# Kernel tuning notes

Measured on AMD Instinct MI355X. Metric: run time of the kernel, lower is better.

## Reference

```python
import jax, jax.numpy as jnp
import numpy as np

NL, NK = 10000, 2000          # ligand / keypoint node counts
ELL, EKL = 320000, 160000     # lig->lig and kp->lig edge counts
IN, HID, OUT = 128, 128, 128  # in_size, hidden_size, out_size
FDIM = 2 * IN + 1             # edge MLP input: [h_src, h_dst, dij]


def silu(x):
    return x * jax.nn.sigmoid(x)


def setup_inputs() -> dict:
    keys = iter(jax.random.split(jax.random.key(0), 64))

    def nrm(shape, scale=0.02):
        return jax.random.normal(next(keys), shape, dtype=jnp.float32) * scale

    d = {}
    d["h_lig"] = jax.random.normal(next(keys), (NL, IN), dtype=jnp.float32)
    d["h_kp"] = jax.random.normal(next(keys), (NK, IN), dtype=jnp.float32)
    d["x_lig"] = jax.random.normal(next(keys), (NL, 3), dtype=jnp.float32)
    d["x_kp"] = jax.random.normal(next(keys), (NK, 3), dtype=jnp.float32)
    # per-node normalizer (e.g. neighbor count); keep >= 1 to avoid blowup
    d["z_lig"] = jax.random.uniform(next(keys), (NL, 1), dtype=jnp.float32, minval=1.0, maxval=32.0)
    for e in ("ll", "kl"):
        d[e + "_eW1"] = nrm((FDIM, HID)); d[e + "_eb1"] = jnp.zeros((HID,), jnp.float32)
        d[e + "_eW2"] = nrm((HID, HID)); d[e + "_eb2"] = jnp.zeros((HID,), jnp.float32)
        d[e + "_aW"] = nrm((HID, 1)); d[e + "_ab"] = jnp.zeros((1,), jnp.float32)
        d[e + "_cW1"] = nrm((FDIM, HID)); d[e + "_cb1"] = jnp.zeros((HID,), jnp.float32)
        d[e + "_cW2"] = nrm((HID, HID)); d[e + "_cb2"] = jnp.zeros((HID,), jnp.float32)
        d[e + "_cW3"] = nrm((HID, 1), scale=0.001)  # xavier gain=0.001 final coord layer
    d["n_W1"] = nrm((IN + HID, HID)); d["n_b1"] = jnp.zeros((HID,), jnp.float32)
    d["n_W2"] = nrm((HID, OUT)); d["n_b2"] = jnp.zeros((OUT,), jnp.float32)
    d["ll_src"] = jax.random.randint(next(keys), (ELL,), 0, NL, dtype=jnp.int32)
    d["ll_dst"] = jax.random.randint(next(keys), (ELL,), 0, NL, dtype=jnp.int32)
    d["kl_src"] = jax.random.randint(next(keys), (EKL,), 0, NK, dtype=jnp.int32)
    d["kl_dst"] = jax.random.randint(next(keys), (EKL,), 0, NL, dtype=jnp.int32)
    return d


def _edge_messages(hs, hd, xs, xd, eW1, eb1, eW2, eb2, aW, ab, cW1, cb1, cW2, cb2, cW3):
    x_diff = xs - xd                                     # fn.u_sub_v
    dij = jnp.linalg.norm(x_diff, axis=1, keepdims=True)  # [E,1]
    x_diff = x_diff / (dij + 1.0)
    f = jnp.concatenate([hs, hd, dij], axis=1)           # [E, 2*IN+1]
    m = silu(f @ eW1 + eb1)
    m = silu(m @ eW2 + eb2)
    msg_h = m * jax.nn.sigmoid(m @ aW + ab)              # soft attention gate
    c = silu(f @ cW1 + cb1)
    c = silu(c @ cW2 + cb2)
    msg_x = (c @ cW3) * x_diff                           # use_tanh=False path
    return msg_h, msg_x


def reference(h_lig, h_kp, x_lig, x_kp, z_lig,
              ll_eW1, ll_eb1, ll_eW2, ll_eb2, ll_aW, ll_ab,
              ll_cW1, ll_cb1, ll_cW2, ll_cb2, ll_cW3,
              kl_eW1, kl_eb1, kl_eW2, kl_eb2, kl_aW, kl_ab,
              kl_cW1, kl_cb1, kl_cW2, kl_cb2, kl_cW3,
              n_W1, n_b1, n_W2, n_b2,
              ll_src, ll_dst, kl_src, kl_dst):
    # lig -> lig edges
    mh_ll, mx_ll = _edge_messages(h_lig[ll_src], h_lig[ll_dst], x_lig[ll_src], x_lig[ll_dst],
                                  ll_eW1, ll_eb1, ll_eW2, ll_eb2, ll_aW, ll_ab,
                                  ll_cW1, ll_cb1, ll_cW2, ll_cb2, ll_cW3)
    # kp -> lig edges
    mh_kl, mx_kl = _edge_messages(h_kp[kl_src], h_lig[kl_dst], x_kp[kl_src], x_lig[kl_dst],
                                  kl_eW1, kl_eb1, kl_eW2, kl_eb2, kl_aW, kl_ab,
                                  kl_cW1, kl_cb1, kl_cW2, kl_cb2, kl_cW3)
    nl = h_lig.shape[0]
    # multi_update_all with cross_reducer='sum', then per-node normalization by z
    h_neigh = (jax.ops.segment_sum(mh_ll, ll_dst, num_segments=nl)
               + jax.ops.segment_sum(mh_kl, kl_dst, num_segments=nl)) / z_lig
    x_neigh = (jax.ops.segment_sum(mx_ll, ll_dst, num_segments=nl)
               + jax.ops.segment_sum(mx_kl, kl_dst, num_segments=nl)) / z_lig
    nin = jnp.concatenate([h_lig, h_neigh], axis=1)
    h_out = h_lig + (silu(nin @ n_W1 + n_b1) @ n_W2 + n_b2)  # norm=False -> Identity
    x_out = x_lig + x_neigh
    return (h_out, x_out)
```

## Files before the change

### kernel.cpp

```cpp
#include <hip/hip_runtime.h>
#include <hip/hip_bf16.h>
#include <math.h>

#define EPB  32
#define MSTR 136
#define FSTR 264

typedef __attribute__((ext_vector_type(8))) short short8;
typedef __attribute__((ext_vector_type(4))) float f32x4;

__device__ __forceinline__ unsigned short f2bf(float x) {
    unsigned int u = __float_as_uint(x);
    u += 0x7fffu + ((u >> 16) & 1u);
    return (unsigned short)(u >> 16);
}
__device__ __forceinline__ float bf2f(short v) {
    return __uint_as_float(((unsigned int)(unsigned short)v) << 16);
}
__device__ __forceinline__ unsigned int pkbf(float a, float b) {
    __hip_bfloat162 h = __float22bfloat162_rn(make_float2(a, b));
    union { __hip_bfloat162 h2; unsigned int u; } cv; cv.h2 = h; return cv.u;
}
__device__ __forceinline__ float frcp(float x) { return __builtin_amdgcn_rcpf(x); }
__device__ __forceinline__ float fsilu(float x) {
    return x * frcp(1.0f + __expf(-x));
}
__device__ __forceinline__ float fsigm(float x) {
    return frcp(1.0f + __expf(-x));
}
__device__ __forceinline__ void atomAddF(float* p, float v) {
    unsafeAtomicAdd(p, v);
}

template<int CTRL>
__device__ __forceinline__ float dppAdd(float x) {
    int y = __builtin_amdgcn_update_dpp(0, __float_as_int(x), CTRL, 0xF, 0xF, false);
    return x + __int_as_float(y);
}
__device__ __forceinline__ float rowSum16(float g) {
    g = dppAdd<0xB1>(g);
    g = dppAdd<0x4E>(g);
    g = dppAdd<0x124>(g);
    g = dppAdd<0x128>(g);
    return g;
}

struct PrepArgs { const float* src[10]; };

__global__ __launch_bounds__(256) void prep_hist_kernel(PrepArgs pa, short* __restrict__ wsb,
                                                        const int* __restrict__ lld,
                                                        const int* __restrict__ kld,
                                                        int* __restrict__ hist,
                                                        float* __restrict__ zfill) {
    int idx = blockIdx.x * 256 + threadIdx.x;
    if (idx < 245760) {
        int pair = idx / 49152;
        int rem  = idx - pair * 49152;
        int second = (rem >= 32768) ? 1 : 0;
        int mi = pair * 2 + second;
        int within = second ? (rem - 32768) : rem;
        int n, k, K;
        if (second) { K = 128; n = within >> 7; k = within & 127; }
        else        { K = 256; n = within >> 8; k = within & 255; }
        int dstoff = pair * 49152 + second * 32768;
        wsb[dstoff + n * K + k] = (short)f2bf(pa.src[mi][k * 128 + n]);
        return;
    }
    idx -= 245760;
    if (idx < 320000) { atomicAdd(&hist[lld[idx]], 1); return; }
    idx -= 320000;
    if (idx < 160000) { atomicAdd(&hist[10000 + kld[idx]], 1); return; }
    idx -= 160000;
    if (idx < 327500)
        ((float4*)zfill)[idx] = make_float4(0.f, 0.f, 0.f, 0.f);
}

struct ProjDesc { const float* A; const short* Bt; short* out; const float* bias;
                  int rows; int ktb; int co; int hasb; };
struct BArgs {
    const int* hist;
    int* cursor;
    ProjDesc d[8];
};

__global__ __launch_bounds__(256) void scan_proj_kernel(BArgs ba) {
    __shared__ __align__(16) short a_lds[64 * MSTR];
    const int t = threadIdx.x;
    if (blockIdx.x < 2) {
        __shared__ int ps[256];
        const int* h = ba.hist + blockIdx.x * 10000;
        int* cur = ba.cursor + blockIdx.x * 10000;
        const int base = t * 40;
        int v[40];
#pragma unroll
        for (int i = 0; i < 40; i++) {
            int ii = base + i;
            v[i] = (ii < 10000) ? h[ii] : 0;
        }
        int s = 0;
#pragma unroll
        for (int i = 0; i < 40; i++) s += v[i];
        ps[t] = s;
        __syncthreads();
        for (int off = 1; off < 256; off <<= 1) {
            int x = (t >= off) ? ps[t - off] : 0;
            __syncthreads();
            ps[t] += x;
            __syncthreads();
        }
        int run = ps[t] - s;
#pragma unroll
        for (int i = 0; i < 40; i++) {
            int ii = base + i;
            if (ii < 10000) { cur[ii] = run; run += v[i]; }
        }
        return;
    }
    const int pb = blockIdx.x - 2;
    const int di = pb / 157, tile = pb - di * 157;
    const ProjDesc pd = ba.d[di];
    if (tile * 64 >= pd.rows) return;
    {
        const int r = t >> 2, q = t & 3;
        const int node = tile * 64 + r;
        short* arow = a_lds + r * MSTR + q * 32;
        if (node < pd.rows) {
            const float* ap = pd.A + (size_t)node * 128 + q * 32;
#pragma unroll
            for (int i = 0; i < 4; i++) {
                float4 v0 = *(const float4*)(ap + i * 8);
                float4 v1 = *(const float4*)(ap + i * 8 + 4);
                uint4 o;
                o.x = pkbf(v0.x, v0.y); o.y = pkbf(v0.z, v0.w);
                o.z = pkbf(v1.x, v1.y); o.w = pkbf(v1.z, v1.w);
                *(uint4*)(arow + i * 8) = o;
            }
        } else {
            uint4 z = make_uint4(0, 0, 0, 0);
#pragma unroll
            for (int i = 0; i < 4; i++) *(uint4*)(arow + i * 8) = z;
        }
    }
    __syncthreads();

    const int ln = t & 63, wv = t >> 6;
    const int lrow = ln & 15, quad = ln >> 4;
    const int c0 = wv * 32 + lrow, c1 = c0 + 16;

    short8 bf0[4], bf1[4];
#pragma unroll
    for (int kt = 0; kt < 4; kt++) {
        bf0[kt] = *(const short8*)(pd.Bt + c0 * 256 + (pd.ktb + kt) * 32 + quad * 8);
        bf1[kt] = *(const short8*)(pd.Bt + c1 * 256 + (pd.ktb + kt) * 32 + quad * 8);
    }
    const float bb0 = pd.hasb ? pd.bias[c0] : 0.0f;
    const float bb1 = pd.hasb ? pd.bias[c1] : 0.0f;
#pragma unroll
    for (int mt = 0; mt < 4; mt++) {
        short8 af[4];
#pragma unroll
        for (int kt = 0; kt < 4; kt++)
            af[kt] = *(const short8*)(&a_lds[(mt * 16 + lrow) * MSTR + kt * 32 + quad * 8]);
        f32x4 a0 = {0.f, 0.f, 0.f, 0.f}, a1 = {0.f, 0.f, 0.f, 0.f};
#pragma unroll
        for (int kt = 0; kt < 4; kt++) {
            a0 = __builtin_amdgcn_mfma_f32_16x16x32_bf16(af[kt], bf0[kt], a0, 0, 0, 0);
            a1 = __builtin_amdgcn_mfma_f32_16x16x32_bf16(af[kt], bf1[kt], a1, 0, 0, 0);
        }
#pragma unroll
        for (int r = 0; r < 4; r++) {
            const int node = tile * 64 + mt * 16 + quad * 4 + r;
            if (node < pd.rows) {
                pd.out[(size_t)node * 256 + pd.co + c0] = (short)f2bf(a0[r] + bb0);
                pd.out[(size_t)node * 256 + pd.co + c1] = (short)f2bf(a1[r] + bb1);
            }
        }
    }
}

struct SArgs {
    const int *lls, *lld, *kls, *kld;
    int* cursor;
    int2 *ll_spk, *kl_spk;
};

__global__ __launch_bounds__(256) void scatter_kernel(SArgs sa) {
    int i = blockIdx.x * 256 + threadIdx.x;
    if (i < 320000) {
        int s = sa.lls[i];
        int d = sa.lld[i];
        int p = atomicAdd(&sa.cursor[d], 1);
        sa.ll_spk[p] = make_int2(s, d);
    } else if (i < 480000) {
        int j = i - 320000;
        int s = sa.kls[j];
        int d = sa.kld[j];
        int p = atomicAdd(&sa.cursor[10000 + d], 1);
        sa.kl_spk[p] = make_int2(s, d);
    }
}

struct EdgeSet {
    const short *Ps, *Pd;
    const float *xs, *xd;
    const int2 *esd;
    const float *w256e, *w256c;
    const short *W2t, *cW2t;
    const float *b2e, *b2c;
    const float *aW, *ab, *cW3;
};
struct EdgePair { EdgeSet s[2]; int split; };

__global__ __launch_bounds__(256, 6) void edge_kernel(EdgePair ep,
                                                      float* __restrict__ hne,
                                                      float* __restrict__ xne)
{
    __shared__ __align__(16) char mbuf[EPB * MSTR * 4];
    __shared__ float sv_l[EPB];
    __shared__ float gate_l[EPB];
    __shared__ float xdf[3][EPB];
    __shared__ int   dstl[EPB];
    __shared__ float gpc[4][EPB];
    __shared__ float gpe[4][EPB];

    short* mh = (short*)mbuf;
    short* mc = (short*)(mbuf + EPB * MSTR * 2);
    float* msg = (float*)mbuf;

    const int isKL = (blockIdx.x >= ep.split) ? 1 : 0;
    const EdgeSet P = ep.s[isKL];
    int b = blockIdx.x - (isKL ? ep.split : 0);
    const int nb8 = isKL ? 625 : 1250;
    b = (b & 7) * nb8 + (b >> 3);
    const int eb = b * EPB;
    const int t = threadIdx.x;

    {
        const int e = t >> 3, q = t & 7;
        const int eid = eb + e;
        const int2 sd = P.esd[eid];
        const int s = sd.x, d = sd.y;
        const short* psrow = P.Ps + (size_t)s * 256 + q * 16;
        const short* pdrow = P.Pd + (size_t)d * 256 + q * 16;
        short8 ra[2][2], rb[2][2];
#pragma unroll
        for (int path = 0; path < 2; path++)
#pragma unroll
            for (int i = 0; i < 2; i++) {
                ra[path][i] = *(const short8*)(psrow + path * 128 + i * 8);
                rb[path][i] = *(const short8*)(pdrow + path * 128 + i * 8);
            }
        float dx = P.xs[s * 3 + 0] - P.xd[d * 3 + 0];
        float dy = P.xs[s * 3 + 1] - P.xd[d * 3 + 1];
        float dz = P.xs[s * 3 + 2] - P.xd[d * 3 + 2];
        float dd = __builtin_amdgcn_sqrtf(dx * dx + dy * dy + dz * dz);
        if (q == 0) {
            dstl[e] = d;
            float inv = frcp(dd + 1.0f);
            xdf[0][e] = dx * inv; xdf[1][e] = dy * inv; xdf[2][e] = dz * inv;
        }
#pragma unroll
        for (int path = 0; path < 2; path++) {
            const float* wq = (path ? P.w256c : P.w256e) + q * 16;
            short* mrow = (path ? mc : mh) + e * MSTR + q * 16;
#pragma unroll
            for (int i = 0; i < 2; i++) {
                short8 a = ra[path][i];
                short8 b2 = rb[path][i];
                float4 wA = *(const float4*)(wq + i * 8);
                float4 wB = *(const float4*)(wq + i * 8 + 4);
                float v0 = fsilu(bf2f(a[0]) + bf2f(b2[0]) + dd * wA.x);
                float v1 = fsilu(bf2f(a[1]) + bf2f(b2[1]) + dd * wA.y);
                float v2 = fsilu(bf2f(a[2]) + bf2f(b2[2]) + dd * wA.z);
                float v3 = fsilu(bf2f(a[3]) + bf2f(b2[3]) + dd * wA.w);
                float v4 = fsilu(bf2f(a[4]) + bf2f(b2[4]) + dd * wB.x);
                float v5 = fsilu(bf2f(a[5]) + bf2f(b2[5]) + dd * wB.y);
                float v6 = fsilu(bf2f(a[6]) + bf2f(b2[6]) + dd * wB.z);
                float v7 = fsilu(bf2f(a[7]) + bf2f(b2[7]) + dd * wB.w);
                uint4 o;
                o.x = pkbf(v0, v1); o.y = pkbf(v2, v3);
                o.z = pkbf(v4, v5); o.w = pkbf(v6, v7);
                *(uint4*)(mrow + i * 8) = o;
            }
        }
    }
    __syncthreads();

    const int ln = t & 63, wv = t >> 6;
    const int lrow = ln & 15, quad = ln >> 4;
    const int c0 = wv * 32 + lrow, c1 = c0 + 16;

    {
        short8 bf0[4], bf1[4];
#pragma unroll
        for (int kt = 0; kt < 4; kt++) {
            bf0[kt] = *(const short8*)(P.cW2t + c0 * 128 + kt * 32 + quad * 8);
            bf1[kt] = *(const short8*)(P.cW2t + c1 * 128 + kt * 32 + quad * 8);
        }
        const float cw0 = P.cW3[c0], cw1 = P.cW3[c1];
        const float bb0 = P.b2c[c0], bb1 = P.b2c[c1];
#pragma unroll
        for (int mt = 0; mt < 2; mt++) {
            short8 af[4];
#pragma unroll
            for (int kt = 0; kt < 4; kt++)
                af[kt] = *(const short8*)(&mc[(mt * 16 + lrow) * MSTR + kt * 32 + quad * 8]);
            f32x4 a0 = {0.f, 0.f, 0.f, 0.f}, a1 = {0.f, 0.f, 0.f, 0.f};
#pragma unroll
            for (int kt = 0; kt < 4; kt++) {
                a0 = __builtin_amdgcn_mfma_f32_16x16x32_bf16(af[kt], bf0[kt], a0, 0, 0, 0);
                a1 = __builtin_amdgcn_mfma_f32_16x16x32_bf16(af[kt], bf1[kt], a1, 0, 0, 0);
            }
#pragma unroll
            for (int r = 0; r < 4; r++) {
                float v0 = fsilu(a0[r] + bb0);
                float v1 = fsilu(a1[r] + bb1);
                float g = rowSum16(v0 * cw0 + v1 * cw1);
                if (lrow == 0) gpc[wv][mt * 16 + quad * 4 + r] = g;
            }
        }
    }

    float m2s[2][8];
    {
        short8 bf0[4], bf1[4];
#pragma unroll
        for (int kt = 0; kt < 4; kt++) {
            bf0[kt] = *(const short8*)(P.W2t + c0 * 128 + kt * 32 + quad * 8);
            bf1[kt] = *(const short8*)(P.W2t + c1 * 128 + kt * 32 + quad * 8);
        }
        const float aw0 = P.aW[c0], aw1 = P.aW[c1];
        const float bb0 = P.b2e[c0], bb1 = P.b2e[c1];
#pragma unroll
        for (int mt = 0; mt < 2; mt++) {
            short8 af[4];
#pragma unroll
            for (int kt = 0; kt < 4; kt++)
                af[kt] = *(const short8*)(&mh[(mt * 16 + lrow) * MSTR + kt * 32 + quad * 8]);
            f32x4 a0 = {0.f, 0.f, 0.f, 0.f}, a1 = {0.f, 0.f, 0.f, 0.f};
#pragma unroll
            for (int kt = 0; kt < 4; kt++) {
                a0 = __builtin_amdgcn_mfma_f32_16x16x32_bf16(af[kt], bf0[kt], a0, 0, 0, 0);
                a1 = __builtin_amdgcn_mfma_f32_16x16x32_bf16(af[kt], bf1[kt], a1, 0, 0, 0);
            }
#pragma unroll
            for (int r = 0; r < 4; r++) {
                float v0 = fsilu(a0[r] + bb0);
                float v1 = fsilu(a1[r] + bb1);
                m2s[mt][r] = v0; m2s[mt][4 + r] = v1;
                float g = rowSum16(v0 * aw0 + v1 * aw1);
                if (lrow == 0) gpe[wv][mt * 16 + quad * 4 + r] = g;
            }
        }
    }
    __syncthreads();

    if (t < EPB) {
        sv_l[t]   = gpc[0][t] + gpc[1][t] + gpc[2][t] + gpc[3][t];
        gate_l[t] = fsigm(gpe[0][t] + gpe[1][t] + gpe[2][t] + gpe[3][t] + P.ab[0]);
    }
#pragma unroll
    for (int mt = 0; mt < 2; mt++)
#pragma unroll
        for (int r = 0; r < 4; r++) {
            const int erow = mt * 16 + quad * 4 + r;
            msg[erow * 132 + c0] = m2s[mt][r];
            msg[erow * 132 + c1] = m2s[mt][4 + r];
        }
    __syncthreads();

    {
        const int col = t & 127;
        const int e0 = (t >> 7) * 16;
        float acc = 0.0f;
        int cur = dstl[e0];
#pragma unroll 4
        for (int e = e0; e < e0 + 16; e++) {
            const int d = dstl[e];
            if (d != cur) {
                atomAddF(&hne[(size_t)cur * 128 + col], acc);
                acc = 0.0f; cur = d;
            }
            acc += msg[e * 132 + col] * gate_l[e];
        }
        atomAddF(&hne[(size_t)cur * 128 + col], acc);
    }
    if (t < 6) {
        const int ax = (t >= 3) ? (t - 3) : t;
        const int e0 = (t >= 3) ? 16 : 0;
        float acc = 0.0f;
        int cur = dstl[e0];
        for (int e = e0; e < e0 + 16; e++) {
            const int d = dstl[e];
            if (d != cur) {
                atomAddF(&xne[cur * 3 + ax], acc);
                acc = 0.0f; cur = d;
            }
            acc += sv_l[e] * xdf[ax][e];
        }
        atomAddF(&xne[cur * 3 + ax], acc);
    }
}

__global__ __launch_bounds__(256) void node_kernel(
    const float* __restrict__ h_lig, const float* __restrict__ zlig,
    const short* __restrict__ W1t, const float* __restrict__ b1v,
    const short* __restrict__ W2t, const float* __restrict__ b2v,
    const float* __restrict__ x_lig,
    const float* __restrict__ acc_h, const float* __restrict__ acc_x,
    float* __restrict__ h_out, float* __restrict__ x_out)
{
    __shared__ __align__(16) short f_lds[64 * FSTR];
    __shared__ __align__(16) short m_lds[64 * MSTR];
    const int t = threadIdx.x;
    const int nb = blockIdx.x * 64;

    {
        const int e = t >> 2, q = t & 3;
        const int node = nb + e;
        short* frow = &f_lds[e * FSTR + q * 32];
        if (node < 10000) {
            const float zi = frcp(zlig[node]);
            const float4* hp = (const float4*)(h_lig + (size_t)node * 128 + q * 32);
            const float4* np = (const float4*)(acc_h + (size_t)node * 128 + q * 32);
#pragma unroll
            for (int i = 0; i < 8; i++) {
                float4 v = hp[i];
                *(uint2*)(frow + i * 4) = make_uint2(pkbf(v.x, v.y), pkbf(v.z, v.w));
            }
#pragma unroll
            for (int i = 0; i < 8; i++) {
                float4 v = np[i];
                *(uint2*)(frow + 128 + i * 4) =
                    make_uint2(pkbf(v.x * zi, v.y * zi), pkbf(v.z * zi, v.w * zi));
            }
        } else {
            const uint2 zz = make_uint2(0, 0);
#pragma unroll
            for (int i = 0; i < 8; i++) {
                *(uint2*)(frow + i * 4) = zz;
                *(uint2*)(frow + 128 + i * 4) = zz;
            }
        }
    }
    __syncthreads();

    const int ln = t & 63, wv = t >> 6;
    const int lrow = ln & 15, quad = ln >> 4;
    const int c0 = wv * 32 + lrow, c1 = c0 + 16;

    {
        short8 bf0[8], bf1[8];
#pragma unroll
        for (int kt = 0; kt < 8; kt++) {
            bf0[kt] = *(const short8*)(W1t + c0 * 256 + kt * 32 + quad * 8);
            bf1[kt] = *(const short8*)(W1t + c1 * 256 + kt * 32 + quad * 8);
        }
        const float bb0 = b1v[c0], bb1 = b1v[c1];
#pragma unroll
        for (int mt = 0; mt < 4; mt++) {
            short8 af[8];
#pragma unroll
            for (int kt = 0; kt < 8; kt++)
                af[kt] = *(const short8*)(&f_lds[(mt * 16 + lrow) * FSTR + kt * 32 + quad * 8]);
            f32x4 a0 = {0.f, 0.f, 0.f, 0.f}, a1 = {0.f, 0.f, 0.f, 0.f};
#pragma unroll
            for (int kt = 0; kt < 8; kt++) {
                a0 = __builtin_amdgcn_mfma_f32_16x16x32_bf16(af[kt], bf0[kt], a0, 0, 0, 0);
                a1 = __builtin_amdgcn_mfma_f32_16x16x32_bf16(af[kt], bf1[kt], a1, 0, 0, 0);
            }
#pragma unroll
            for (int r = 0; r < 4; r++) {
                const int erow = mt * 16 + quad * 4 + r;
                m_lds[erow * MSTR + c0] = (short)f2bf(fsilu(a0[r] + bb0));
                m_lds[erow * MSTR + c1] = (short)f2bf(fsilu(a1[r] + bb1));
            }
        }
    }
    __syncthreads();

    {
        short8 bf0[4], bf1[4];
#pragma unroll
        for (int kt = 0; kt < 4; kt++) {
            bf0[kt] = *(const short8*)(W2t + c0 * 128 + kt * 32 + quad * 8);
            bf1[kt] = *(const short8*)(W2t + c1 * 128 + kt * 32 + quad * 8);
        }
        const float bb0 = b2v[c0], bb1 = b2v[c1];
#pragma unroll
        for (int mt = 0; mt < 4; mt++) {
            short8 af[4];
#pragma unroll
            for (int kt = 0; kt < 4; kt++)
                af[kt] = *(const short8*)(&m_lds[(mt * 16 + lrow) * MSTR + kt * 32 + quad * 8]);
            f32x4 a0 = {0.f, 0.f, 0.f, 0.f}, a1 = {0.f, 0.f, 0.f, 0.f};
#pragma unroll
            for (int kt = 0; kt < 4; kt++) {
                a0 = __builtin_amdgcn_mfma_f32_16x16x32_bf16(af[kt], bf0[kt], a0, 0, 0, 0);
                a1 = __builtin_amdgcn_mfma_f32_16x16x32_bf16(af[kt], bf1[kt], a1, 0, 0, 0);
            }
#pragma unroll
            for (int r = 0; r < 4; r++) {
                const int node = nb + mt * 16 + quad * 4 + r;
                if (node < 10000) {
                    h_out[(size_t)node * 128 + c0] = a0[r] + bb0 + h_lig[(size_t)node * 128 + c0];
                    h_out[(size_t)node * 128 + c1] = a1[r] + bb1 + h_lig[(size_t)node * 128 + c1];
                }
            }
        }
    }
    if (t < 64) {
        const int node = nb + t;
        if (node < 10000) {
            const float zi = frcp(zlig[node]);
#pragma unroll
            for (int i = 0; i < 3; i++)
                x_out[node * 3 + i] = x_lig[node * 3 + i] + acc_x[node * 3 + i] * zi;
        }
    }
}

extern "C" void kernel_launch(void* const* d_in, const int* in_sizes, int n_in,
                              void* d_out, int out_size, void* d_ws, size_t ws_size,
                              hipStream_t stream)
{
    (void)in_sizes; (void)n_in; (void)ws_size; (void)out_size;
    const float* h_lig  = (const float*)d_in[0];
    const float* h_kp   = (const float*)d_in[1];
    const float* x_lig  = (const float*)d_in[2];
    const float* x_kp   = (const float*)d_in[3];
    const float* z_lig  = (const float*)d_in[4];
    const float* ll_eW1 = (const float*)d_in[5];
    const float* ll_eb1 = (const float*)d_in[6];
    const float* ll_eW2 = (const float*)d_in[7];
    const float* ll_eb2 = (const float*)d_in[8];
    const float* ll_aW  = (const float*)d_in[9];
    const float* ll_ab  = (const float*)d_in[10];
    const float* ll_cW1 = (const float*)d_in[11];
    const float* ll_cb1 = (const float*)d_in[12];
    const float* ll_cW2 = (const float*)d_in[13];
    const float* ll_cb2 = (const float*)d_in[14];
    const float* ll_cW3 = (const float*)d_in[15];
    const float* kl_eW1 = (const float*)d_in[16];
    const float* kl_eb1 = (const float*)d_in[17];
    const float* kl_eW2 = (const float*)d_in[18];
    const float* kl_eb2 = (const float*)d_in[19];
    const float* kl_aW  = (const float*)d_in[20];
    const float* kl_ab  = (const float*)d_in[21];
    const float* kl_cW1 = (const float*)d_in[22];
    const float* kl_cb1 = (const float*)d_in[23];
    const float* kl_cW2 = (const float*)d_in[24];
    const float* kl_cb2 = (const float*)d_in[25];
    const float* kl_cW3 = (const float*)d_in[26];
    const float* n_W1   = (const float*)d_in[27];
    const float* n_b1   = (const float*)d_in[28];
    const float* n_W2   = (const float*)d_in[29];
    const float* n_b2   = (const float*)d_in[30];
    const int* ll_src = (const int*)d_in[31];
    const int* ll_dst = (const int*)d_in[32];
    const int* kl_src = (const int*)d_in[33];
    const int* kl_dst = (const int*)d_in[34];

    float* h_out = (float*)d_out;
    float* x_out = h_out + 1280000;

    char* wsc = (char*)d_ws;
    short* wsb    = (short*)wsc;
    short* P_ll_s = (short*)(wsc +   491520);
    short* P_ll_d = (short*)(wsc +  5611520);
    short* P_kl_s = (short*)(wsc + 10731520);
    short* P_kl_d = (short*)(wsc + 11755520);
    int2* ll_spk  = (int2*)(wsc + 16875520);
    int2* kl_spk  = (int2*)(wsc + 19435520);
    int* hist     = (int*)(wsc + 20715520);
    int* cursor   = (int*)(wsc + 20795520);
    float* hne    = (float*)(wsc + 20875520);
    float* xne    = (float*)(wsc + 25995520);

    (void)hipMemsetAsync(hist, 0, 80000, stream);

    {
        PrepArgs pa;
        pa.src[0] = ll_eW1; pa.src[1] = ll_eW2; pa.src[2] = ll_cW1; pa.src[3] = ll_cW2;
        pa.src[4] = kl_eW1; pa.src[5] = kl_eW2; pa.src[6] = kl_cW1; pa.src[7] = kl_cW2;
        pa.src[8] = n_W1;   pa.src[9] = n_W2;
        prep_hist_kernel<<<4115, 256, 0, stream>>>(pa, wsb, ll_dst, kl_dst, hist, hne);
    }
    {
        BArgs ba;
        ba.hist = hist; ba.cursor = cursor;
        ba.d[0] = { h_lig, wsb + 0,      P_ll_s, ll_eb1, 10000, 0, 0,   0 };
        ba.d[1] = { h_lig, wsb + 49152,  P_ll_s, ll_cb1, 10000, 0, 128, 0 };
        ba.d[2] = { h_lig, wsb + 0,      P_ll_d, ll_eb1, 10000, 4, 0,   1 };
        ba.d[3] = { h_lig, wsb + 49152,  P_ll_d, ll_cb1, 10000, 4, 128, 1 };
        ba.d[4] = { h_kp,  wsb + 98304,  P_kl_s, kl_eb1,  2000, 0, 0,   0 };
        ba.d[5] = { h_kp,  wsb + 147456, P_kl_s, kl_cb1,  2000, 0, 128, 0 };
        ba.d[6] = { h_lig, wsb + 98304,  P_kl_d, kl_eb1, 10000, 4, 0,   1 };
        ba.d[7] = { h_lig, wsb + 147456, P_kl_d, kl_cb1, 10000, 4, 128, 1 };
        scan_proj_kernel<<<2 + 8 * 157, 256, 0, stream>>>(ba);
    }
    {
        SArgs sa;
        sa.lls = ll_src; sa.lld = ll_dst; sa.kls = kl_src; sa.kld = kl_dst;
        sa.cursor = cursor;
        sa.ll_spk = ll_spk; sa.kl_spk = kl_spk;
        scatter_kernel<<<1875, 256, 0, stream>>>(sa);
    }
    {
        EdgePair ep;
        ep.split = 10000;
        ep.s[0] = { P_ll_s, P_ll_d, x_lig, x_lig, ll_spk,
                    ll_eW1 + 256 * 128, ll_cW1 + 256 * 128,
                    wsb + 32768, wsb + 81920, ll_eb2, ll_cb2,
                    ll_aW, ll_ab, ll_cW3 };
        ep.s[1] = { P_kl_s, P_kl_d, x_kp, x_lig, kl_spk,
                    kl_eW1 + 256 * 128, kl_cW1 + 256 * 128,
                    wsb + 131072, wsb + 180224, kl_eb2, kl_cb2,
                    kl_aW, kl_ab, kl_cW3 };
        edge_kernel<<<15000, 256, 0, stream>>>(ep, hne, xne);
    }
    node_kernel<<<157, 256, 0, stream>>>(
        h_lig, z_lig, wsb + 196608, n_b1, wsb + 229376, n_b2,
        x_lig, hne, xne, h_out, x_out);
}
```

Baseline: 373.8 us.

## Double edges per block to 64 with 512 threads and packed bf16 SiLU

Each edge_kernel block now handles 64 edges instead of 32 and launches 512 threads, half the previous grid. The eight waves split into two halves that each run the MFMA layers on 32 edge rows. The block-to-XCD remap is generalised to handle block counts not divisible by 8. The first-layer SiLU now works on packed pairs of bf16 values without staging the gathered loads in registers first. The aim is to amortise per-block setup and the per-destination atomic flushes over more edges, at the cost of a stricter launch-bounds hint that may limit registers or occupancy.

```diff
diff --git a/kernel.cpp b/kernel.cpp
--- a/kernel.cpp
+++ b/kernel.cpp
@@ -2,12 +2,14 @@
 #include <hip/hip_bf16.h>
 #include <math.h>
 
-#define EPB  32
+#define EPB  64
 #define MSTR 136
 #define FSTR 264
 
 typedef __attribute__((ext_vector_type(8))) short short8;
 typedef __attribute__((ext_vector_type(4))) float f32x4;
+typedef __attribute__((ext_vector_type(2))) float f32x2;
+typedef __attribute__((ext_vector_type(4))) unsigned int u32x4;
 
 __device__ __forceinline__ unsigned short f2bf(float x) {
     unsigned int u = __float_as_uint(x);
@@ -27,6 +29,22 @@
 }
 __device__ __forceinline__ float fsigm(float x) {
     return frcp(1.0f + __expf(-x));
+}
+__device__ __forceinline__ f32x2 bfp2f(unsigned int u) {
+    f32x2 r;
+    r.x = __uint_as_float(u << 16);
+    r.y = __uint_as_float(u & 0xffff0000u);
+    return r;
+}
+__device__ __forceinline__ f32x2 silu2(f32x2 x) {
+    f32x2 e;
+    e.x = __expf(-x.x);
+    e.y = __expf(-x.y);
+    f32x2 d = e + (f32x2){1.0f, 1.0f};
+    f32x2 r;
+    r.x = frcp(d.x);
+    r.y = frcp(d.y);
+    return x * r;
 }
 __device__ __forceinline__ void atomAddF(float* p, float v) {
     unsafeAtomicAdd(p, v);
@@ -211,7 +229,7 @@
 };
 struct EdgePair { EdgeSet s[2]; int split; };
 
-__global__ __launch_bounds__(256, 6) void edge_kernel(EdgePair ep,
+__global__ __launch_bounds__(512, 8) void edge_kernel(EdgePair ep,
                                                       float* __restrict__ hne,
                                                       float* __restrict__ xne)
 {
@@ -230,8 +248,12 @@
     const int isKL = (blockIdx.x >= ep.split) ? 1 : 0;
     const EdgeSet P = ep.s[isKL];
     int b = blockIdx.x - (isKL ? ep.split : 0);
-    const int nb8 = isKL ? 625 : 1250;
-    b = (b & 7) * nb8 + (b >> 3);
+    {
+        const int nb = isKL ? 2500 : 5000;
+        const int q8 = nb >> 3, r8 = nb & 7;
+        const int xcd = b & 7, bi = b >> 3;
+        b = (xcd < r8 ? xcd * (q8 + 1) : r8 * (q8 + 1) + (xcd - r8) * q8) + bi;
+    }
     const int eb = b * EPB;
     const int t = threadIdx.x;
 
@@ -242,14 +264,6 @@
         const int s = sd.x, d = sd.y;
         const short* psrow = P.Ps + (size_t)s * 256 + q * 16;
         const short* pdrow = P.Pd + (size_t)d * 256 + q * 16;
-        short8 ra[2][2], rb[2][2];
-#pragma unroll
-        for (int path = 0; path < 2; path++)
-#pragma unroll
-            for (int i = 0; i < 2; i++) {
-                ra[path][i] = *(const short8*)(psrow + path * 128 + i * 8);
-                rb[path][i] = *(const short8*)(pdrow + path * 128 + i * 8);
-            }
         float dx = P.xs[s * 3 + 0] - P.xd[d * 3 + 0];
         float dy = P.xs[s * 3 + 1] - P.xd[d * 3 + 1];
         float dz = P.xs[s * 3 + 2] - P.xd[d * 3 + 2];
@@ -259,27 +273,28 @@
             float inv = frcp(dd + 1.0f);
             xdf[0][e] = dx * inv; xdf[1][e] = dy * inv; xdf[2][e] = dz * inv;
         }
+        const f32x2 dd2 = {dd, dd};
 #pragma unroll
         for (int path = 0; path < 2; path++) {
+            const short* ps = psrow + path * 128;
+            const short* pq = pdrow + path * 128;
             const float* wq = (path ? P.w256c : P.w256e) + q * 16;
             short* mrow = (path ? mc : mh) + e * MSTR + q * 16;
 #pragma unroll
             for (int i = 0; i < 2; i++) {
-                short8 a = ra[path][i];
-                short8 b2 = rb[path][i];
-                float4 wA = *(const float4*)(wq + i * 8);
-                float4 wB = *(const float4*)(wq + i * 8 + 4);
-                float v0 = fsilu(bf2f(a[0]) + bf2f(b2[0]) + dd * wA.x);
-                float v1 = fsilu(bf2f(a[1]) + bf2f(b2[1]) + dd * wA.y);
-                float v2 = fsilu(bf2f(a[2]) + bf2f(b2[2]) + dd * wA.z);
-                float v3 = fsilu(bf2f(a[3]) + bf2f(b2[3]) + dd * wA.w);
-                float v4 = fsilu(bf2f(a[4]) + bf2f(b2[4]) + dd * wB.x);
-                float v5 = fsilu(bf2f(a[5]) + bf2f(b2[5]) + dd * wB.y);
-                float v6 = fsilu(bf2f(a[6]) + bf2f(b2[6]) + dd * wB.z);
-                float v7 = fsilu(bf2f(a[7]) + bf2f(b2[7]) + dd * wB.w);
+                const u32x4 a  = *(const u32x4*)(ps + i * 8);
+                const u32x4 bb = *(const u32x4*)(pq + i * 8);
+                const float4 wA = *(const float4*)(wq + i * 8);
+                const float4 wB = *(const float4*)(wq + i * 8 + 4);
+                const f32x2 w01 = {wA.x, wA.y}, w23 = {wA.z, wA.w};
+                const f32x2 w45 = {wB.x, wB.y}, w67 = {wB.z, wB.w};
+                f32x2 v0 = silu2(bfp2f(a[0]) + bfp2f(bb[0]) + dd2 * w01);
+                f32x2 v1 = silu2(bfp2f(a[1]) + bfp2f(bb[1]) + dd2 * w23);
+                f32x2 v2 = silu2(bfp2f(a[2]) + bfp2f(bb[2]) + dd2 * w45);
+                f32x2 v3 = silu2(bfp2f(a[3]) + bfp2f(bb[3]) + dd2 * w67);
                 uint4 o;
-                o.x = pkbf(v0, v1); o.y = pkbf(v2, v3);
-                o.z = pkbf(v4, v5); o.w = pkbf(v6, v7);
+                o.x = pkbf(v0.x, v0.y); o.y = pkbf(v1.x, v1.y);
+                o.z = pkbf(v2.x, v2.y); o.w = pkbf(v3.x, v3.y);
                 *(uint4*)(mrow + i * 8) = o;
             }
         }
@@ -287,8 +302,11 @@
     __syncthreads();
 
     const int ln = t & 63, wv = t >> 6;
+    const int half = wv >> 2;
+    const int cw = wv & 3;
     const int lrow = ln & 15, quad = ln >> 4;
-    const int c0 = wv * 32 + lrow, c1 = c0 + 16;
+    const int c0 = cw * 32 + lrow, c1 = c0 + 16;
+    const int ebase = half * 32;
 
     {
         short8 bf0[4], bf1[4];
@@ -304,7 +322,7 @@
             short8 af[4];
 #pragma unroll
             for (int kt = 0; kt < 4; kt++)
-                af[kt] = *(const short8*)(&mc[(mt * 16 + lrow) * MSTR + kt * 32 + quad * 8]);
+                af[kt] = *(const short8*)(&mc[(ebase + mt * 16 + lrow) * MSTR + kt * 32 + quad * 8]);
             f32x4 a0 = {0.f, 0.f, 0.f, 0.f}, a1 = {0.f, 0.f, 0.f, 0.f};
 #pragma unroll
             for (int kt = 0; kt < 4; kt++) {
@@ -316,7 +334,7 @@
                 float v0 = fsilu(a0[r] + bb0);
                 float v1 = fsilu(a1[r] + bb1);
                 float g = rowSum16(v0 * cw0 + v1 * cw1);
-                if (lrow == 0) gpc[wv][mt * 16 + quad * 4 + r] = g;
+                if (lrow == 0) gpc[cw][ebase + mt * 16 + quad * 4 + r] = g;
             }
         }
     }
@@ -336,7 +354,7 @@
             short8 af[4];
 #pragma unroll
             for (int kt = 0; kt < 4; kt++)
-                af[kt] = *(const short8*)(&mh[(mt * 16 + lrow) * MSTR + kt * 32 + quad * 8]);
+                af[kt] = *(const short8*)(&mh[(ebase + mt * 16 + lrow) * MSTR + kt * 32 + quad * 8]);
             f32x4 a0 = {0.f, 0.f, 0.f, 0.f}, a1 = {0.f, 0.f, 0.f, 0.f};
 #pragma unroll
             for (int kt = 0; kt < 4; kt++) {
@@ -349,7 +367,7 @@
                 float v1 = fsilu(a1[r] + bb1);
                 m2s[mt][r] = v0; m2s[mt][4 + r] = v1;
                 float g = rowSum16(v0 * aw0 + v1 * aw1);
-                if (lrow == 0) gpe[wv][mt * 16 + quad * 4 + r] = g;
+                if (lrow == 0) gpe[cw][ebase + mt * 16 + quad * 4 + r] = g;
             }
         }
     }
@@ -363,7 +381,7 @@
     for (int mt = 0; mt < 2; mt++)
 #pragma unroll
         for (int r = 0; r < 4; r++) {
-            const int erow = mt * 16 + quad * 4 + r;
+            const int erow = ebase + mt * 16 + quad * 4 + r;
             msg[erow * 132 + c0] = m2s[mt][r];
             msg[erow * 132 + c1] = m2s[mt][4 + r];
         }
@@ -371,7 +389,8 @@
 
     {
         const int col = t & 127;
-        const int e0 = (t >> 7) * 16;
+        const int g = t >> 7;
+        const int e0 = g * 16;
         float acc = 0.0f;
         int cur = dstl[e0];
 #pragma unroll 4
@@ -385,9 +404,10 @@
         }
         atomAddF(&hne[(size_t)cur * 128 + col], acc);
     }
-    if (t < 6) {
-        const int ax = (t >= 3) ? (t - 3) : t;
-        const int e0 = (t >= 3) ? 16 : 0;
+    if (t < 12) {
+        const int g = t / 3;
+        const int ax = t - g * 3;
+        const int e0 = g * 16;
         float acc = 0.0f;
         int cur = dstl[e0];
         for (int e = e0; e < e0 + 16; e++) {
@@ -608,7 +628,7 @@
     }
     {
         EdgePair ep;
-        ep.split = 10000;
+        ep.split = 5000;
         ep.s[0] = { P_ll_s, P_ll_d, x_lig, x_lig, ll_spk,
                     ll_eW1 + 256 * 128, ll_cW1 + 256 * 128,
                     wsb + 32768, wsb + 81920, ll_eb2, ll_cb2,
@@ -617,7 +637,7 @@
                     kl_eW1 + 256 * 128, kl_cW1 + 256 * 128,
                     wsb + 131072, wsb + 180224, kl_eb2, kl_cb2,
                     kl_aW, kl_ab, kl_cW3 };
-        edge_kernel<<<15000, 256, 0, stream>>>(ep, hne, xne);
+        edge_kernel<<<7500, 512, 0, stream>>>(ep, hne, xne);
     }
     node_kernel<<<157, 256, 0, stream>>>(
         h_lig, z_lig, wsb + 196608, n_b1, wsb + 229376, n_b2,
```

After: 384.0 us. 2.7% more time.
